# Optimization experiments

Hardware: AMD Instinct MI355X
Metric: run time of the kernel (lower is better)

## Reference

```python
import jax, jax.numpy as jnp
import numpy as np

N_HEAD = 16
N_EMBD = 1024
BLOCK = 2048
B, T = 4, 2048


def setup_inputs() -> dict:
    key = jax.random.key(0)
    ks = jax.random.split(key, 5)
    scale = 1.0 / np.sqrt(N_EMBD)
    return {
        "x": jax.random.normal(ks[0], (B, T, N_EMBD), dtype=jnp.float32),
        "W_attn": jax.random.normal(ks[1], (N_EMBD, 3 * N_EMBD), dtype=jnp.float32) * scale,
        "b_attn": jax.random.normal(ks[2], (3 * N_EMBD,), dtype=jnp.float32) * 0.02,
        "W_proj": jax.random.normal(ks[3], (N_EMBD, N_EMBD), dtype=jnp.float32) * scale,
        "b_proj": jax.random.normal(ks[4], (N_EMBD,), dtype=jnp.float32) * 0.02,
    }


def reference(x, W_attn, b_attn, W_proj, b_proj):
    Bb, Tt, C = x.shape
    hd = C // N_HEAD
    qkv = x @ W_attn + b_attn                      # [B,T,3C]
    q, k, v = jnp.split(qkv, 3, axis=2)
    # [B,H,T,hd]
    q = q.reshape(Bb, Tt, N_HEAD, hd).transpose(0, 2, 1, 3)
    k = k.reshape(Bb, Tt, N_HEAD, hd).transpose(0, 2, 1, 3)
    v = v.reshape(Bb, Tt, N_HEAD, hd).transpose(0, 2, 1, 3)
    att = jnp.einsum('bhqd,bhkd->bhqk', q, k) / np.sqrt(hd).astype(x.dtype)
    causal = jnp.tril(jnp.ones((Tt, Tt), dtype=bool))
    att = jnp.where(causal[None, None], att, jnp.finfo(att.dtype).min)
    att = jax.nn.softmax(att, axis=-1)
    y = jnp.einsum('bhqk,bhkd->bhqd', att, v)      # [B,H,T,hd]
    y = y.transpose(0, 2, 1, 3).reshape(Bb, Tt, C)
    return y @ W_proj + b_proj
```

## Files before the change

kernel.cpp:

```cpp
#include <hip/hip_runtime.h>
#include <stdint.h>

typedef unsigned short u16;
typedef __bf16 bf16;
typedef bf16 bf16x8 __attribute__((ext_vector_type(8)));
typedef float f32x4 __attribute__((ext_vector_type(4)));
typedef u16 u16x8 __attribute__((ext_vector_type(8)));
typedef u16 u16x4 __attribute__((ext_vector_type(4)));

#define T_SEQ 2048
#define NHEAD 16
#define HD    64
#define CEMB  1024
#define QS    8388608
#define QSCALE 0.18033688011112042f

#define BARRIER() asm volatile("s_barrier" ::: "memory")
#define WAITV(N)  asm volatile("s_waitcnt vmcnt(" #N ")" ::: "memory")

__device__ __forceinline__ u16 f2b(float f){
  bf16 h = (bf16)f;
  return __builtin_bit_cast(u16, h);
}
__device__ __forceinline__ void glds16(const void* g, const void* l){
  __builtin_amdgcn_global_load_lds(
    (__attribute__((address_space(1))) unsigned int*)(uintptr_t)g,
    (__attribute__((address_space(3))) unsigned int*)(uintptr_t)l,
    16, 0, 0);
}

__global__ __launch_bounds__(256) void prep_kernel(
    const float* __restrict__ x, u16* __restrict__ xb,
    const float* __restrict__ Wa, u16* __restrict__ Wta,
    const float* __restrict__ Wp, u16* __restrict__ Wtp)
{
  __shared__ __align__(16) u16 tile[64][72];
  const int bid = blockIdx.x;
  const int tid = threadIdx.x;
  if (bid < 4096){
    const int i = (bid * 256 + tid) * 8;
    f32x4 a = *(const f32x4*)&x[i];
    f32x4 b = *(const f32x4*)&x[i + 4];
    u16x8 h;
    #pragma unroll
    for (int j = 0; j < 4; j++){ h[j] = f2b(a[j]); h[4+j] = f2b(b[j]); }
    *(u16x8*)&xb[i] = h;
    return;
  }
  const float* src; u16* dst; int K, N, bx, by;
  if (bid < 4864){ const int j = bid - 4096; src = Wa; dst = Wta; K = 1024; N = 3072; bx = j % 48; by = j / 48; }
  else           { const int j = bid - 4864; src = Wp; dst = Wtp; K = 1024; N = 1024; bx = j % 16; by = j / 16; }
  const int n0 = bx * 64, k0 = by * 64;
  #pragma unroll
  for (int it = 0; it < 4; it++){
    const int idx = it * 256 + tid;
    const int row = idx >> 4, c4 = (idx & 15) * 4;
    f32x4 v = *(const f32x4*)&src[(size_t)(k0 + row) * N + n0 + c4];
    #pragma unroll
    for (int j = 0; j < 4; j++) tile[row][c4 + j] = f2b(v[j]);
  }
  __syncthreads();
  const int r = tid >> 3, cc = (tid & 7) * 8;
  #pragma unroll
  for (int i = 0; i < 2; i++){
    const int rr = r + i * 32;
    u16x8 v;
    #pragma unroll
    for (int j = 0; j < 8; j++) v[j] = tile[cc + j][rr];
    *(u16x8*)&dst[(size_t)(n0 + rr) * K + k0 + cc] = v;
  }
}

__global__ __launch_bounds__(256) void gemm_qkv128(
    const u16* __restrict__ A, const u16* __restrict__ Bt,
    const float* __restrict__ bias, u16* __restrict__ out, int Ktot)
{
  __shared__ __align__(16) u16 As[128*64];
  __shared__ __align__(16) u16 Bs[128*64];
  const int tid = threadIdx.x;
  const int lane = tid & 63, wave = tid >> 6;
  const int l15 = lane & 15, l4 = lane >> 4;
  const int wm = wave >> 1, wn = wave & 1;
  const int m0 = blockIdx.y * 128, n0 = blockIdx.x * 128;

  f32x4 acc[4][4] = {};

  for (int k0 = 0; k0 < Ktot; k0 += 64){
    #pragma unroll
    for (int ii = 0; ii < 4; ii++){
      const int slot0 = (wave*4 + ii) * 64;
      const int s = slot0 + lane;
      const int row = s >> 3;
      const int c = (s & 7) ^ (row & 7);
      glds16(&A [(size_t)(m0 + row) * Ktot + k0 + c*8], &As[slot0*8]);
      glds16(&Bt[(size_t)(n0 + row) * Ktot + k0 + c*8], &Bs[slot0*8]);
    }
    __syncthreads();
    #pragma unroll
    for (int ks = 0; ks < 2; ks++){
      bf16x8 af[4], bfr[4];
      #pragma unroll
      for (int mt = 0; mt < 4; mt++){
        const int rf = wm*64 + mt*16 + l15;
        const int slot = rf*8 + ((ks*4 + l4) ^ (rf & 7));
        af[mt] = *(const bf16x8*)&As[slot*8];
      }
      #pragma unroll
      for (int nt = 0; nt < 4; nt++){
        const int rf = wn*64 + nt*16 + l15;
        const int slot = rf*8 + ((ks*4 + l4) ^ (rf & 7));
        bfr[nt] = *(const bf16x8*)&Bs[slot*8];
      }
      #pragma unroll
      for (int mt = 0; mt < 4; mt++)
        #pragma unroll
        for (int nt = 0; nt < 4; nt++)
          acc[mt][nt] = __builtin_amdgcn_mfma_f32_16x16x32_bf16(
              af[mt], bfr[nt], acc[mt][nt], 0, 0, 0);
    }
    __syncthreads();
  }

  #pragma unroll
  for (int nt = 0; nt < 4; nt++){
    const int n = n0 + wn*64 + nt*16 + l15;
    const float bias_v = bias[n];
    const int which = n >> 10;
    const int cc = n & 1023;
    const int h = cc >> 6, d = cc & 63;
    const float sc = (which == 0) ? QSCALE : 1.0f;
    if (which == 2){
      #pragma unroll
      for (int mt = 0; mt < 4; mt++){
        const int rowg = m0 + wm*64 + mt*16 + l4*4;
        const int bb = rowg >> 11, t = rowg & 2047;
        u16x4 pk;
        #pragma unroll
        for (int r = 0; r < 4; r++) pk[r] = f2b(acc[mt][nt][r] + bias_v);
        *(u16x4*)&out[(size_t)2*QS + ((size_t)(bb*NHEAD + h)*HD + d)*T_SEQ + t] = pk;
      }
    } else {
      #pragma unroll
      for (int mt = 0; mt < 4; mt++)
        #pragma unroll
        for (int r = 0; r < 4; r++){
          const int rowg = m0 + wm*64 + mt*16 + l4*4 + r;
          const int bb = rowg >> 11, t = rowg & 2047;
          out[(size_t)which*QS + ((size_t)(bb*NHEAD + h)*T_SEQ + t)*HD + d]
              = f2b((acc[mt][nt][r] + bias_v) * sc);
        }
    }
  }
}

__global__ __launch_bounds__(256) void gemm_proj(
    const u16* __restrict__ A, const u16* __restrict__ Bt,
    const float* __restrict__ bias, float* __restrict__ out, int Ktot)
{
  __shared__ __align__(16) u16 As[128*64];
  __shared__ __align__(16) u16 Bs[128*64];
  const int tid = threadIdx.x;
  const int lane = tid & 63, wave = tid >> 6;
  const int l15 = lane & 15, l4 = lane >> 4;
  const int wm = wave >> 1, wn = wave & 1;
  const int m0 = blockIdx.y * 128, n0 = blockIdx.x * 128;

  f32x4 acc[4][4] = {};

  for (int k0 = 0; k0 < Ktot; k0 += 64){
    #pragma unroll
    for (int ii = 0; ii < 4; ii++){
      const int slot0 = (wave*4 + ii) * 64;
      const int s = slot0 + lane;
      const int row = s >> 3;
      const int c = (s & 7) ^ (row & 7);
      glds16(&A [(size_t)(m0 + row) * Ktot + k0 + c*8], &As[slot0*8]);
      glds16(&Bt[(size_t)(n0 + row) * Ktot + k0 + c*8], &Bs[slot0*8]);
    }
    __syncthreads();
    #pragma unroll
    for (int ks = 0; ks < 2; ks++){
      bf16x8 af[4], bfr[4];
      #pragma unroll
      for (int mt = 0; mt < 4; mt++){
        const int rf = wm*64 + mt*16 + l15;
        const int slot = rf*8 + ((ks*4 + l4) ^ (rf & 7));
        af[mt] = *(const bf16x8*)&As[slot*8];
      }
      #pragma unroll
      for (int nt = 0; nt < 4; nt++){
        const int rf = wn*64 + nt*16 + l15;
        const int slot = rf*8 + ((ks*4 + l4) ^ (rf & 7));
        bfr[nt] = *(const bf16x8*)&Bs[slot*8];
      }
      #pragma unroll
      for (int mt = 0; mt < 4; mt++)
        #pragma unroll
        for (int nt = 0; nt < 4; nt++)
          acc[mt][nt] = __builtin_amdgcn_mfma_f32_16x16x32_bf16(
              af[mt], bfr[nt], acc[mt][nt], 0, 0, 0);
    }
    __syncthreads();
  }

  #pragma unroll
  for (int nt = 0; nt < 4; nt++){
    const int n = n0 + wn*64 + nt*16 + l15;
    const float bias_v = bias[n];
    #pragma unroll
    for (int mt = 0; mt < 4; mt++)
      #pragma unroll
      for (int r = 0; r < 4; r++){
        const int rowg = m0 + wm*64 + mt*16 + l4*4 + r;
        out[(size_t)rowg*CEMB + n] = acc[mt][nt][r] + bias_v;
      }
  }
}

__global__ __launch_bounds__(256, 3) void attn_kernel(
    const u16* __restrict__ qb, const u16* __restrict__ kb,
    const u16* __restrict__ vtb, u16* __restrict__ y)
{
  __shared__ __align__(16) u16 Ks[2*64*64];
  __shared__ __align__(16) u16 Vt[2*64*64];
  __shared__ __align__(16) u16 Pw[8*16*72];
  const int tid = threadIdx.x;
  const int lane = tid & 63, wave = tid >> 6;
  const int l15 = lane & 15, l4 = lane >> 4;
  const int qt = 15 - (blockIdx.x >> 6);
  const int bh = blockIdx.x & 63;
  const int q0 = qt * 128;
  const size_t base = (size_t)bh * (T_SEQ * HD);
  const u16* qp  = qb  + base;
  const u16* kp  = kb  + base;
  const u16* vtp = vtb + base;

  const int qmin0 = q0 + wave*32;
  const int qmin1 = qmin0 + 16;

  bf16x8 qf[2][2];
  #pragma unroll
  for (int g = 0; g < 2; g++){
    const int m = qmin0 + g*16 + l15;
    qf[g][0] = *(const bf16x8*)&qp[m*HD +      l4*8];
    qf[g][1] = *(const bf16x8*)&qp[m*HD + 32 + l4*8];
  }
  f32x4 o[2][4] = {};
  float l_run[2] = {0.f, 0.f};

  const int s0i = (wave*2 + 0) * 64 + lane;
  const int s1i = (wave*2 + 1) * 64 + lane;
  const int row0 = s0i >> 3, c0 = (s0i & 7) ^ (row0 & 7);
  const int row1 = s1i >> 3, c1 = (s1i & 7) ^ (row1 & 7);
  const int koff0 = row0*HD + c0*8, koff1 = row1*HD + c1*8;
  const int voff0 = row0*T_SEQ + c0*8, voff1 = row1*T_SEQ + c1*8;
  const int ldso0 = (wave*2 + 0) * 64 * 8, ldso1 = (wave*2 + 1) * 64 * 8;

  const int nkt = 2*qt + 2;

  glds16(&kp [koff0], &Ks[ldso0]);
  glds16(&kp [koff1], &Ks[ldso1]);
  glds16(&vtp[voff0], &Vt[ldso0]);
  glds16(&vtp[voff1], &Vt[ldso1]);

  for (int kt = 0; kt < nkt; kt++){
    const int cb = (kt & 1) * 4096;
    if (kt + 1 < nkt){
      const int nb = ((kt + 1) & 1) * 4096;
      glds16(&kp [(kt+1)*4096 + koff0], &Ks[nb + ldso0]);
      glds16(&kp [(kt+1)*4096 + koff1], &Ks[nb + ldso1]);
      glds16(&vtp[(kt+1)*64   + voff0], &Vt[nb + ldso0]);
      glds16(&vtp[(kt+1)*64   + voff1], &Vt[nb + ldso1]);
      WAITV(4);
    } else {
      WAITV(0);
    }
    BARRIER();

    const int t0 = kt*64;
    if (t0 <= qmin1 + 15){
      const bool act0 = (t0 <= qmin0 + 15);

      f32x4 s0[4], s1[4];
      #pragma unroll
      for (int nb2 = 0; nb2 < 4; nb2++){
        f32x4 a0 = {}, a1 = {};
        #pragma unroll
        for (int ks = 0; ks < 2; ks++){
          const int rf = nb2*16 + l15;
          const int slot = rf*8 + ((ks*4 + l4) ^ (rf & 7));
          bf16x8 kf = *(const bf16x8*)&Ks[cb + slot*8];
          a1 = __builtin_amdgcn_mfma_f32_16x16x32_bf16(kf, qf[1][ks], a1, 0, 0, 0);
          if (act0)
            a0 = __builtin_amdgcn_mfma_f32_16x16x32_bf16(kf, qf[0][ks], a0, 0, 0, 0);
        }
        s1[nb2] = a1; s0[nb2] = a0;
      }

      #pragma unroll
      for (int g = 0; g < 2; g++){
        if (g == 0 && !act0) continue;
        f32x4* sf = (g == 0) ? s0 : s1;
        const int qmin = (g == 0) ? qmin0 : qmin1;
        const int qg = qmin + l15;
        float lsum = 0.f;
        if (t0 + 63 > qmin){
          #pragma unroll
          for (int nb2 = 0; nb2 < 4; nb2++){
            u16x4 pk;
            #pragma unroll
            for (int r = 0; r < 4; r++){
              const int t = t0 + nb2*16 + l4*4 + r;
              float p = __builtin_amdgcn_exp2f(sf[nb2][r]);
              p = (t <= qg) ? p : 0.0f;
              lsum += p;
              pk[r] = f2b(p);
            }
            *(u16x4*)&Pw[(wave*2 + g)*1152 + l15*72 + nb2*16 + l4*4] = pk;
          }
        } else {
          #pragma unroll
          for (int nb2 = 0; nb2 < 4; nb2++){
            u16x4 pk;
            #pragma unroll
            for (int r = 0; r < 4; r++){
              const float p = __builtin_amdgcn_exp2f(sf[nb2][r]);
              lsum += p;
              pk[r] = f2b(p);
            }
            *(u16x4*)&Pw[(wave*2 + g)*1152 + l15*72 + nb2*16 + l4*4] = pk;
          }
        }
        l_run[g] += lsum;
      }

      #pragma unroll
      for (int ks = 0; ks < 2; ks++){
        bf16x8 pf1 = *(const bf16x8*)&Pw[(wave*2 + 1)*1152 + l15*72 + ks*32 + l4*8];
        bf16x8 pf0;
        if (act0) pf0 = *(const bf16x8*)&Pw[(wave*2 + 0)*1152 + l15*72 + ks*32 + l4*8];
        #pragma unroll
        for (int nh = 0; nh < 4; nh++){
          const int rf = nh*16 + l15;
          const int slot = rf*8 + ((ks*4 + l4) ^ (rf & 7));
          bf16x8 vf = *(const bf16x8*)&Vt[cb + slot*8];
          o[1][nh] = __builtin_amdgcn_mfma_f32_16x16x32_bf16(vf, pf1, o[1][nh], 0, 0, 0);
          if (act0)
            o[0][nh] = __builtin_amdgcn_mfma_f32_16x16x32_bf16(vf, pf0, o[0][nh], 0, 0, 0);
        }
      }
    }
    BARRIER();
  }

  const int b = bh >> 4, h = bh & 15;
  #pragma unroll
  for (int g = 0; g < 2; g++){
    float lr = l_run[g];
    lr += __shfl_xor(lr, 16);
    lr += __shfl_xor(lr, 32);
    const float inv_l = 1.0f / lr;
    const int t = qmin0 + g*16 + l15;
    #pragma unroll
    for (int nh = 0; nh < 4; nh++){
      u16x4 pk;
      #pragma unroll
      for (int r = 0; r < 4; r++) pk[r] = f2b(o[g][nh][r] * inv_l);
      *(u16x4*)&y[((size_t)(b*T_SEQ + t))*CEMB + h*HD + nh*16 + l4*4] = pk;
    }
  }
}

extern "C" void kernel_launch(void* const* d_in, const int* in_sizes, int n_in,
                              void* d_out, int out_size, void* d_ws, size_t ws_size,
                              hipStream_t stream) {
  const float* x      = (const float*)d_in[0];
  const float* W_attn = (const float*)d_in[1];
  const float* b_attn = (const float*)d_in[2];
  const float* W_proj = (const float*)d_in[3];
  const float* b_proj = (const float*)d_in[4];
  float* out = (float*)d_out;
  u16* ws  = (u16*)d_ws;

  u16* Wt_attn = ws;
  u16* Wt_proj = ws + 3145728;
  u16* xb      = ws + 4194304;
  u16* qkv     = ws + 12582912;
  u16* y       = xb;

  prep_kernel<<<5120, 256, 0, stream>>>(x, xb, W_attn, Wt_attn, W_proj, Wt_proj);
  gemm_qkv128<<<dim3(24, 64), 256, 0, stream>>>(xb, Wt_attn, b_attn, qkv, 1024);
  attn_kernel<<<1024, 256, 0, stream>>>(qkv, qkv + QS, qkv + 2*QS, y);
  gemm_proj<<<dim3(8, 64), 256, 0, stream>>>(y, Wt_proj, b_proj, out, 1024);
}
```

Before: 238.1 us.

## Double-buffer LDS tiles in QKV and proj GEMMs with swizzled block order

Both GEMM kernels now keep two LDS buffers and issue the global-to-LDS loads for the next K tile before computing on the current one. Explicit vmcnt waits and raw barriers replace __syncthreads, so load latency can overlap with MFMA work. Blocks are also remapped from a 1D grid in an interleaved order, meant to improve L2 reuse across the 8 XCDs. LDS use per block doubles, which may lower occupancy, and the hand-counted vmcnt value must match the number of outstanding loads.

```diff
diff --git a/kernel.cpp b/kernel.cpp
--- a/kernel.cpp
+++ b/kernel.cpp
@@ -71,31 +71,46 @@
   }
 }
 
+#define QSTAGE(BUF, K0) do{ \
+  _Pragma("unroll") \
+  for (int ii = 0; ii < 4; ii++){ \
+    const int slot0 = (wave*4 + ii) * 64; \
+    const int s = slot0 + lane; \
+    const int row = s >> 3; \
+    const int cc8 = ((s & 7) ^ (row & 7)) * 8; \
+    glds16(&A [(size_t)(m0 + row) * Ktot + (K0) + cc8], &As[BUF][slot0*8]); \
+    glds16(&Bt[(size_t)(n0 + row) * Ktot + (K0) + cc8], &Bs[BUF][slot0*8]); \
+  } \
+}while(0)
+
 __global__ __launch_bounds__(256) void gemm_qkv128(
     const u16* __restrict__ A, const u16* __restrict__ Bt,
     const float* __restrict__ bias, u16* __restrict__ out, int Ktot)
 {
-  __shared__ __align__(16) u16 As[128*64];
-  __shared__ __align__(16) u16 Bs[128*64];
+  __shared__ __align__(16) u16 As[2][128*64];
+  __shared__ __align__(16) u16 Bs[2][128*64];
   const int tid = threadIdx.x;
   const int lane = tid & 63, wave = tid >> 6;
   const int l15 = lane & 15, l4 = lane >> 4;
   const int wm = wave >> 1, wn = wave & 1;
-  const int m0 = blockIdx.y * 128, n0 = blockIdx.x * 128;
+  const int id = blockIdx.x;
+  const int swz = (id & 7) * 192 + (id >> 3);
+  const int m0 = (swz / 24) * 128, n0 = (swz % 24) * 128;
+  const int NT = Ktot >> 6;
 
   f32x4 acc[4][4] = {};
 
-  for (int k0 = 0; k0 < Ktot; k0 += 64){
-    #pragma unroll
-    for (int ii = 0; ii < 4; ii++){
-      const int slot0 = (wave*4 + ii) * 64;
-      const int s = slot0 + lane;
-      const int row = s >> 3;
-      const int c = (s & 7) ^ (row & 7);
-      glds16(&A [(size_t)(m0 + row) * Ktot + k0 + c*8], &As[slot0*8]);
-      glds16(&Bt[(size_t)(n0 + row) * Ktot + k0 + c*8], &Bs[slot0*8]);
-    }
-    __syncthreads();
+  QSTAGE(0, 0);
+  for (int c = 0; c < NT; c++){
+    const int cur = c & 1;
+    if (c + 1 < NT){
+      QSTAGE(cur ^ 1, (c + 1) * 64);
+      WAITV(8);
+    } else {
+      WAITV(0);
+    }
+    BARRIER();
+
     #pragma unroll
     for (int ks = 0; ks < 2; ks++){
       bf16x8 af[4], bfr[4];
@@ -103,13 +118,13 @@
       for (int mt = 0; mt < 4; mt++){
         const int rf = wm*64 + mt*16 + l15;
         const int slot = rf*8 + ((ks*4 + l4) ^ (rf & 7));
-        af[mt] = *(const bf16x8*)&As[slot*8];
+        af[mt] = *(const bf16x8*)&As[cur][slot*8];
       }
       #pragma unroll
       for (int nt = 0; nt < 4; nt++){
         const int rf = wn*64 + nt*16 + l15;
         const int slot = rf*8 + ((ks*4 + l4) ^ (rf & 7));
-        bfr[nt] = *(const bf16x8*)&Bs[slot*8];
+        bfr[nt] = *(const bf16x8*)&Bs[cur][slot*8];
       }
       #pragma unroll
       for (int mt = 0; mt < 4; mt++)
@@ -118,7 +133,7 @@
           acc[mt][nt] = __builtin_amdgcn_mfma_f32_16x16x32_bf16(
               af[mt], bfr[nt], acc[mt][nt], 0, 0, 0);
     }
-    __syncthreads();
+    BARRIER();
   }
 
   #pragma unroll
@@ -157,27 +172,30 @@
     const u16* __restrict__ A, const u16* __restrict__ Bt,
     const float* __restrict__ bias, float* __restrict__ out, int Ktot)
 {
-  __shared__ __align__(16) u16 As[128*64];
-  __shared__ __align__(16) u16 Bs[128*64];
+  __shared__ __align__(16) u16 As[2][128*64];
+  __shared__ __align__(16) u16 Bs[2][128*64];
   const int tid = threadIdx.x;
   const int lane = tid & 63, wave = tid >> 6;
   const int l15 = lane & 15, l4 = lane >> 4;
   const int wm = wave >> 1, wn = wave & 1;
-  const int m0 = blockIdx.y * 128, n0 = blockIdx.x * 128;
+  const int id = blockIdx.x;
+  const int swz = (id & 7) * 64 + (id >> 3);
+  const int m0 = (swz / 8) * 128, n0 = (swz % 8) * 128;
+  const int NT = Ktot >> 6;
 
   f32x4 acc[4][4] = {};
 
-  for (int k0 = 0; k0 < Ktot; k0 += 64){
-    #pragma unroll
-    for (int ii = 0; ii < 4; ii++){
-      const int slot0 = (wave*4 + ii) * 64;
-      const int s = slot0 + lane;
-      const int row = s >> 3;
-      const int c = (s & 7) ^ (row & 7);
-      glds16(&A [(size_t)(m0 + row) * Ktot + k0 + c*8], &As[slot0*8]);
-      glds16(&Bt[(size_t)(n0 + row) * Ktot + k0 + c*8], &Bs[slot0*8]);
-    }
-    __syncthreads();
+  QSTAGE(0, 0);
+  for (int c = 0; c < NT; c++){
+    const int cur = c & 1;
+    if (c + 1 < NT){
+      QSTAGE(cur ^ 1, (c + 1) * 64);
+      WAITV(8);
+    } else {
+      WAITV(0);
+    }
+    BARRIER();
+
     #pragma unroll
     for (int ks = 0; ks < 2; ks++){
       bf16x8 af[4], bfr[4];
@@ -185,13 +203,13 @@
       for (int mt = 0; mt < 4; mt++){
         const int rf = wm*64 + mt*16 + l15;
         const int slot = rf*8 + ((ks*4 + l4) ^ (rf & 7));
-        af[mt] = *(const bf16x8*)&As[slot*8];
+        af[mt] = *(const bf16x8*)&As[cur][slot*8];
       }
       #pragma unroll
       for (int nt = 0; nt < 4; nt++){
         const int rf = wn*64 + nt*16 + l15;
         const int slot = rf*8 + ((ks*4 + l4) ^ (rf & 7));
-        bfr[nt] = *(const bf16x8*)&Bs[slot*8];
+        bfr[nt] = *(const bf16x8*)&Bs[cur][slot*8];
       }
       #pragma unroll
       for (int mt = 0; mt < 4; mt++)
@@ -200,7 +218,7 @@
           acc[mt][nt] = __builtin_amdgcn_mfma_f32_16x16x32_bf16(
               af[mt], bfr[nt], acc[mt][nt], 0, 0, 0);
     }
-    __syncthreads();
+    BARRIER();
   }
 
   #pragma unroll
@@ -389,7 +407,7 @@
   u16* y       = xb;
 
   prep_kernel<<<5120, 256, 0, stream>>>(x, xb, W_attn, Wt_attn, W_proj, Wt_proj);
-  gemm_qkv128<<<dim3(24, 64), 256, 0, stream>>>(xb, Wt_attn, b_attn, qkv, 1024);
+  gemm_qkv128<<<1536, 256, 0, stream>>>(xb, Wt_attn, b_attn, qkv, 1024);
   attn_kernel<<<1024, 256, 0, stream>>>(qkv, qkv + QS, qkv + 2*QS, y);
-  gemm_proj<<<dim3(8, 64), 256, 0, stream>>>(y, Wt_proj, b_proj, out, 1024);
-}
+  gemm_proj<<<512, 256, 0, stream>>>(y, Wt_proj, b_proj, out, 1024);
+}
```

Measured after the change: 226.9 us. -4.7%, faster.
